# Kernel optimization log

Measured on AMD Instinct MI355X. Metric: run time of the kernel, lower is better.

## Reference

```python
import math
import jax, jax.numpy as jnp
import numpy as np

D = 4  # BWGNN d


def calculate_theta2(d):
    # Faithful numeric reimplementation of the sympy version.
    # f_i(x) = (x/2)^i (1-x/2)^(d-i) / (2*Beta(i+1, d+1-i)); the original code
    # keeps only the d lowest-order (ascending) coefficients, dropping x^d.
    thetas = []
    for i in range(d):
        c1 = np.zeros(i + 1); c1[i] = 0.5 ** i                      # (x/2)^i
        c2 = np.array([math.comb(d - i, j) * (-0.5) ** j
                       for j in range(d - i + 1)])                   # (1-x/2)^(d-i)
        c = np.convolve(c1, c2)                                      # ascending, len d+1
        B = math.factorial(i) * math.factorial(d - i) / math.factorial(d + 1)
        c = c / (2.0 * B)
        thetas.append([float(c[j]) for j in range(d)])               # coeff[d-i] slicing
    return thetas

THETAS = calculate_theta2(D)


def setup_inputs() -> dict:
    key = jax.random.key(0)
    k1, k2, k3, k4 = jax.random.split(key, 4)
    N, E, F_in, H = 100000, 1600000, 128, 64
    feature = jax.random.normal(k1, (N, F_in), dtype=jnp.float32)
    edge_index = jax.random.randint(k2, (2, E), 0, N, dtype=jnp.int32)
    W = jax.random.normal(k3, (F_in, H), dtype=jnp.float32) * 0.05
    b = jax.random.normal(k4, (H,), dtype=jnp.float32) * 0.05
    return {"feature": feature, "edge_index": edge_index, "W": W, "b": b}


def reference(feature, edge_index, W, b):
    N = feature.shape[0]
    src, dst = edge_index[0], edge_index[1]
    # out_degrees: number of out-edges per node (src side), clamped to >= 1
    deg = jax.ops.segment_sum(jnp.ones_like(src, dtype=jnp.float32), src,
                              num_segments=N)
    D_invsqrt = jnp.maximum(deg, 1.0) ** -0.5  # [N]
    D_invsqrt = D_invsqrt[:, None]             # [N,1]

    h = jax.nn.leaky_relu(feature @ W + b, negative_slope=0.01)  # [N,H]

    def unn_laplacian(feat):
        # feat - D^{-1/2} A^T D^{-1/2} feat  (copy_u + sum over dst)
        msg = (feat * D_invsqrt)[src]                          # [E,H]
        agg = jax.ops.segment_sum(msg, dst, num_segments=N)    # [N,H]
        return feat - agg * D_invsqrt

    outs = []
    for theta in THETAS:
        feat = h
        acc = theta[0] * feat
        for k in range(1, len(theta)):
            feat = unn_laplacian(feat)
            acc = acc + theta[k] * feat
        outs.append(acc)
    return jnp.concatenate(outs, axis=1)  # [N, len(THETAS)*H]
```

## Files before the change

kernel.cpp:

```cpp
#include <hip/hip_runtime.h>

#define THREADS 256
#define ELLW 64
#define T1 4096
#define BCAP 8192
#define NBMAX 512

__device__ __forceinline__ float bf2f(unsigned short u) {
    return __uint_as_float(((unsigned int)u) << 16);
}
__device__ __forceinline__ unsigned short f2bf(float x) {
    unsigned int u = __float_as_uint(x);
    u += 0x7fffu + ((u >> 16) & 1u);
    return (unsigned short)(u >> 16);
}

__global__ void bin_kernel(const int* __restrict__ key, const int* __restrict__ val,
                           int* __restrict__ gFill, unsigned int* __restrict__ gBuf, int E) {
    __shared__ int cnt[NBMAX], scanB[NBMAX], gbase[NBMAX], place[NBMAX];
    __shared__ unsigned int stage[T1];
    __shared__ unsigned int stageAddr[T1];
    const int tid = threadIdx.x;
    const int tileStart = blockIdx.x * T1;
    const int tileCnt = min(T1, E - tileStart);

    for (int i = tid; i < NBMAX; i += THREADS) { cnt[i] = 0; place[i] = 0; }
    __syncthreads();

    for (int i = tid; i < tileCnt; i += THREADS)
        atomicAdd(&cnt[key[tileStart + i] >> 8], 1);
    __syncthreads();

    if (tid < 64) {
        const int base = tid * 8;
        int loc[8]; int s = 0;
        #pragma unroll
        for (int k = 0; k < 8; ++k) { loc[k] = s; s += cnt[base + k]; }
        int run = s;
        #pragma unroll
        for (int off = 1; off < 64; off <<= 1) {
            int t = __shfl_up(run, off);
            if (tid >= off) run += t;
        }
        const int excl = run - s;
        #pragma unroll
        for (int k = 0; k < 8; ++k) scanB[base + k] = excl + loc[k];
    }
    __syncthreads();

    for (int i = tid; i < NBMAX; i += THREADS)
        gbase[i] = atomicAdd(&gFill[i], cnt[i]);
    __syncthreads();

    for (int i = tid; i < tileCnt; i += THREADS) {
        const int kk = key[tileStart + i];
        const int vv = val[tileStart + i];
        const int b = kk >> 8;
        const unsigned int rec = ((unsigned int)(kk & 255) << 17) | (unsigned int)vv;
        const int pos = atomicAdd(&place[b], 1);
        const int li = scanB[b] + pos;
        const int gi = gbase[b] + pos;
        stage[li] = rec;
        stageAddr[li] = (gi < BCAP) ? (unsigned int)(b * BCAP + gi) : 0xFFFFFFFFu;
    }
    __syncthreads();

    for (int i = tid; i < tileCnt; i += THREADS) {
        const unsigned int a = stageAddr[i];
        if (a != 0xFFFFFFFFu) gBuf[a] = stage[i];
    }
}

__global__ void ell_kernel(const int* __restrict__ gFill, const unsigned int* __restrict__ gBuf,
                           int* __restrict__ ell, int* __restrict__ fill, int N) {
    __shared__ int ellT[256 * ELLW];
    __shared__ int fillT[256];
    const int tid = threadIdx.x;
    const int b = blockIdx.x;
    const int nrec = min(gFill[b], BCAP);
    for (int i = tid; i < 256; i += THREADS) fillT[i] = 0;
    __syncthreads();
    for (int i = tid; i < nrec; i += THREADS) {
        const unsigned int rec = gBuf[(size_t)b * BCAP + i];
        const int dlow = rec >> 17;
        const int s = rec & 0x1FFFF;
        const int pos = atomicAdd(&fillT[dlow], 1);
        if (pos < ELLW) ellT[dlow * ELLW + pos] = s;
    }
    __syncthreads();
    const int node0 = b << 8;
    const int nvalid = min(256, N - node0);
    if (nvalid <= 0) return;
    for (int t = tid; t < nvalid; t += THREADS) fill[node0 + t] = min(fillT[t], ELLW);
    int4* dstp = (int4*)(ell + (size_t)node0 * ELLW);
    const int4* srcp = (const int4*)ellT;
    for (int i = tid; i < nvalid * 16; i += THREADS) dstp[i] = srcp[i];
}

__global__ void deg_kernel2(const int* __restrict__ gFill, const unsigned int* __restrict__ gBuf,
                            int* __restrict__ deg, int N) {
    __shared__ int cntT[256];
    const int tid = threadIdx.x;
    const int b = blockIdx.x;
    const int nrec = min(gFill[b], BCAP);
    for (int i = tid; i < 256; i += THREADS) cntT[i] = 0;
    __syncthreads();
    for (int i = tid; i < nrec; i += THREADS)
        atomicAdd(&cntT[gBuf[(size_t)b * BCAP + i] >> 17], 1);
    __syncthreads();
    const int node0 = b << 8;
    const int nvalid = min(256, N - node0);
    for (int t = tid; t < nvalid; t += THREADS) deg[node0 + t] = cntT[t];
}

__global__ void build_kernel(const int* __restrict__ src, const int* __restrict__ dst,
                             int* __restrict__ deg, int* __restrict__ fill,
                             int* __restrict__ ell, int E) {
    const int stride = gridDim.x * blockDim.x;
    for (int i = blockIdx.x * blockDim.x + threadIdx.x; i < E; i += stride) {
        const int s = src[i];
        const int d = dst[i];
        atomicAdd(&deg[s], 1);
        const int pos = atomicAdd(&fill[d], 1);
        if (pos < ELLW) ell[(size_t)d * ELLW + pos] = s;
    }
}

__global__ void gemm_leaky(const float* __restrict__ feat, const float* __restrict__ W,
                           const float* __restrict__ b, const int* __restrict__ deg,
                           float* __restrict__ out, int N) {
    __shared__ float Wl[128 * 64];
    __shared__ float fl[64][132];
    __shared__ float bl[64];

    {
        const float4* W4 = (const float4*)W;
        float4* Wl4 = (float4*)Wl;
        for (int i = threadIdx.x; i < 2048; i += THREADS) Wl4[i] = W4[i];
        if (threadIdx.x < 64) bl[threadIdx.x] = b[threadIdx.x];
    }

    const int cg = threadIdx.x & 15;
    const int rg = threadIdx.x >> 4;
    const int ntiles = (N + 63) >> 6;
    char* base = (char*)out;

    for (int tile = blockIdx.x; tile < ntiles; tile += gridDim.x) {
        const int n0 = tile << 6;
        __syncthreads();
        for (int i = threadIdx.x; i < 2048; i += THREADS) {
            int rr = i >> 5;
            int kk = i & 31;
            float4 v = make_float4(0.f, 0.f, 0.f, 0.f);
            if (n0 + rr < N) v = ((const float4*)(feat + (size_t)(n0 + rr) * 128))[kk];
            *((float4*)&fl[rr][kk * 4]) = v;
        }
        __syncthreads();

        float acc[4][4];
        #pragma unroll
        for (int j = 0; j < 4; ++j) {
            float bv = bl[cg * 4 + j];
            acc[0][j] = bv; acc[1][j] = bv; acc[2][j] = bv; acc[3][j] = bv;
        }

        #pragma unroll 4
        for (int k = 0; k < 128; ++k) {
            const float4 w = *((const float4*)&Wl[k * 64 + cg * 4]);
            const float f0 = fl[rg * 4 + 0][k];
            const float f1 = fl[rg * 4 + 1][k];
            const float f2 = fl[rg * 4 + 2][k];
            const float f3 = fl[rg * 4 + 3][k];
            acc[0][0] += f0 * w.x; acc[0][1] += f0 * w.y; acc[0][2] += f0 * w.z; acc[0][3] += f0 * w.w;
            acc[1][0] += f1 * w.x; acc[1][1] += f1 * w.y; acc[1][2] += f1 * w.z; acc[1][3] += f1 * w.w;
            acc[2][0] += f2 * w.x; acc[2][1] += f2 * w.y; acc[2][2] += f2 * w.z; acc[2][3] += f2 * w.w;
            acc[3][0] += f3 * w.x; acc[3][1] += f3 * w.y; acc[3][2] += f3 * w.z; acc[3][3] += f3 * w.w;
        }

        #pragma unroll
        for (int i = 0; i < 4; ++i) {
            const int n = n0 + rg * 4 + i;
            if (n < N) {
                const float dv = rsqrtf(fmaxf((float)deg[n], 1.0f));
                ushort4 o;
                float v0 = acc[i][0] > 0.f ? acc[i][0] : 0.01f * acc[i][0];
                float v1 = acc[i][1] > 0.f ? acc[i][1] : 0.01f * acc[i][1];
                float v2 = acc[i][2] > 0.f ? acc[i][2] : 0.01f * acc[i][2];
                float v3 = acc[i][3] > 0.f ? acc[i][3] : 0.01f * acc[i][3];
                o.x = f2bf(v0 * dv); o.y = f2bf(v1 * dv); o.z = f2bf(v2 * dv); o.w = f2bf(v3 * dv);
                *((ushort4*)(base + (size_t)n * 1024 + cg * 8)) = o;
            }
        }
    }
}

__global__ void hop_kernel(const int* __restrict__ ell, const int* __restrict__ fill,
                           const int* __restrict__ deg, float* __restrict__ out,
                           int N, int prevOff, int nextOff) {
    const int lane = threadIdx.x & 63;
    const int nwaves = (gridDim.x * blockDim.x) >> 6;
    char* base = (char*)out;
    for (int n = (blockIdx.x * blockDim.x + threadIdx.x) >> 6; n < N; n += nwaves) {
        const int cnt = min(fill[n], ELLW);
        const int c = ell[(size_t)n * ELLW + lane];
        float acc = 0.0f;
        int j = 0;
        for (; j + 4 <= cnt; j += 4) {
            const int s0 = __shfl(c, j);
            const int s1 = __shfl(c, j + 1);
            const int s2 = __shfl(c, j + 2);
            const int s3 = __shfl(c, j + 3);
            const float v0 = bf2f(*(const unsigned short*)(base + (size_t)s0 * 1024 + prevOff + lane * 2));
            const float v1 = bf2f(*(const unsigned short*)(base + (size_t)s1 * 1024 + prevOff + lane * 2));
            const float v2 = bf2f(*(const unsigned short*)(base + (size_t)s2 * 1024 + prevOff + lane * 2));
            const float v3 = bf2f(*(const unsigned short*)(base + (size_t)s3 * 1024 + prevOff + lane * 2));
            acc += (v0 + v1) + (v2 + v3);
        }
        for (; j < cnt; ++j) {
            const int s = __shfl(c, j);
            acc += bf2f(*(const unsigned short*)(base + (size_t)s * 1024 + prevOff + lane * 2));
        }
        const float own = bf2f(*(const unsigned short*)(base + (size_t)n * 1024 + prevOff + lane * 2));
        const float d = fmaxf((float)deg[n], 1.0f);
        const float sn = own - acc / d;
        *(unsigned short*)(base + (size_t)n * 1024 + nextOff + lane * 2) = f2bf(sn);
    }
}

__global__ void combine_kernel(float* __restrict__ out, const int* __restrict__ deg, int N) {
    const int lane = threadIdx.x & 63;
    const int nwaves = (gridDim.x * blockDim.x) >> 6;
    char* base = (char*)out;
    for (int n = (blockIdx.x * blockDim.x + threadIdx.x) >> 6; n < N; n += nwaves) {
        char* row = base + (size_t)n * 1024;
        const float s0 = bf2f(*(const unsigned short*)(row + 0   + lane * 2));
        const float s1 = bf2f(*(const unsigned short*)(row + 128 + lane * 2));
        const float s2 = bf2f(*(const unsigned short*)(row + 256 + lane * 2));
        const float s3 = bf2f(*(const unsigned short*)(row + 384 + lane * 2));
        const float sc = sqrtf(fmaxf((float)deg[n], 1.0f));
        const float h  = s0 * sc;
        const float p1 = s1 * sc;
        const float p2 = s2 * sc;
        const float p3 = s3 * sc;
        const float o0 = 2.5f * h - 5.0f * p1 + 3.75f * p2 - 1.25f * p3;
        const float o1 = 5.0f * p1 - 7.5f * p2 + 3.75f * p3;
        const float o2 = 3.75f * (p2 - p3);
        const float o3 = 1.25f * p3;
        float* frow = (float*)row;
        frow[lane]       = o0;
        frow[64 + lane]  = o1;
        frow[128 + lane] = o2;
        frow[192 + lane] = o3;
    }
}

extern "C" void kernel_launch(void* const* d_in, const int* in_sizes, int n_in,
                              void* d_out, int out_size, void* d_ws, size_t ws_size,
                              hipStream_t stream) {
    const float* feature = (const float*)d_in[0];
    const int*   eidx    = (const int*)d_in[1];
    const float* W       = (const float*)d_in[2];
    const float* b       = (const float*)d_in[3];
    float* out = (float*)d_out;

    const int N = in_sizes[0] / 128;
    const int E = in_sizes[1] / 2;
    const int* src = eidx;
    const int* dst = eidx + E;

    const int nb = (N + 255) >> 8;

    int* deg    = (int*)d_ws;
    int* fill   = deg + N;
    int* ell    = fill + N;
    int* gFillD = ell + (size_t)N * ELLW;
    int* gFillS = gFillD + NBMAX;
    unsigned int* gBufD = (unsigned int*)(gFillS + NBMAX);
    unsigned int* gBufS = gBufD + (size_t)nb * BCAP;

    if (N <= 131072) {
        hipMemsetAsync(gFillD, 0, 2 * NBMAX * sizeof(int), stream);
        const int tiles = (E + T1 - 1) / T1;
        bin_kernel<<<tiles, THREADS, 0, stream>>>(dst, src, gFillD, gBufD, E);
        bin_kernel<<<tiles, THREADS, 0, stream>>>(src, src, gFillS, gBufS, E);
        ell_kernel<<<nb, THREADS, 0, stream>>>(gFillD, gBufD, ell, fill, N);
        deg_kernel2<<<nb, THREADS, 0, stream>>>(gFillS, gBufS, deg, N);
    } else {
        hipMemsetAsync(deg, 0, (size_t)2 * N * sizeof(int), stream);
        build_kernel<<<2048, THREADS, 0, stream>>>(src, dst, deg, fill, ell, E);
    }

    const int gemm_blocks = (N + 63) / 64;
    gemm_leaky<<<gemm_blocks, THREADS, 0, stream>>>(feature, W, b, deg, out, N);

    const int gblocks = (N + 3) / 4;
    hop_kernel<<<gblocks, THREADS, 0, stream>>>(ell, fill, deg, out, N, 0, 128);
    hop_kernel<<<gblocks, THREADS, 0, stream>>>(ell, fill, deg, out, N, 128, 256);
    hop_kernel<<<gblocks, THREADS, 0, stream>>>(ell, fill, deg, out, N, 256, 384);

    combine_kernel<<<gblocks, THREADS, 0, stream>>>(out, deg, N);
}
```

Before: 269.4 us.

## Replace fixed-width ELL adjacency with compact CSR built via block scans

New measurement: 288.4 us. 1.07x slower.

```diff
diff --git a/kernel.cpp b/kernel.cpp
--- a/kernel.cpp
+++ b/kernel.cpp
@@ -1,7 +1,6 @@
 #include <hip/hip_runtime.h>
 
 #define THREADS 256
-#define ELLW 64
 #define T1 4096
 #define BCAP 8192
 #define NBMAX 512
@@ -13,6 +12,11 @@
     unsigned int u = __float_as_uint(x);
     u += 0x7fffu + ((u >> 16) & 1u);
     return (unsigned short)(u >> 16);
+}
+
+__global__ void zero_kernel(int* __restrict__ p, int n) {
+    const int i = blockIdx.x * blockDim.x + threadIdx.x;
+    if (i < n) p[i] = 0;
 }
 
 __global__ void bin_kernel(const int* __restrict__ key, const int* __restrict__ val,
@@ -71,30 +75,68 @@
     }
 }
 
-__global__ void ell_kernel(const int* __restrict__ gFill, const unsigned int* __restrict__ gBuf,
-                           int* __restrict__ ell, int* __restrict__ fill, int N) {
-    __shared__ int ellT[256 * ELLW];
-    __shared__ int fillT[256];
+__global__ void scanb_kernel(const int* __restrict__ gFill, int* __restrict__ gBase,
+                             int* __restrict__ rowptr, int nb, int N) {
+    __shared__ int s[NBMAX];
+    const int tid = threadIdx.x;
+    const int v = (tid < nb) ? min(gFill[tid], BCAP) : 0;
+    s[tid] = v;
+    __syncthreads();
+    for (int off = 1; off < NBMAX; off <<= 1) {
+        int t = (tid >= off) ? s[tid - off] : 0;
+        __syncthreads();
+        s[tid] += t;
+        __syncthreads();
+    }
+    if (tid < nb) gBase[tid] = s[tid] - v;
+    if (tid == NBMAX - 1) rowptr[N] = s[NBMAX - 1];
+}
+
+__global__ void csr_kernel(const int* __restrict__ gFill, const int* __restrict__ gBase,
+                           const unsigned int* __restrict__ gBuf,
+                           int* __restrict__ rowptr, int* __restrict__ col, int N) {
+    __shared__ int fillT[256], offT[256], place[256], sc[256];
+    __shared__ int colT[BCAP];
+    __shared__ int nwrite;
     const int tid = threadIdx.x;
     const int b = blockIdx.x;
     const int nrec = min(gFill[b], BCAP);
-    for (int i = tid; i < 256; i += THREADS) fillT[i] = 0;
-    __syncthreads();
+    const int base = gBase[b];
+
+    fillT[tid] = 0; place[tid] = 0;
+    __syncthreads();
+    for (int i = tid; i < nrec; i += THREADS)
+        atomicAdd(&fillT[gBuf[(size_t)b * BCAP + i] >> 17], 1);
+    __syncthreads();
+
+    int v = fillT[tid];
+    sc[tid] = v;
+    __syncthreads();
+    for (int off = 1; off < 256; off <<= 1) {
+        int t = (tid >= off) ? sc[tid - off] : 0;
+        __syncthreads();
+        sc[tid] += t;
+        __syncthreads();
+    }
+    offT[tid] = sc[tid] - v;
+    if (tid == 255) nwrite = sc[255];
+    __syncthreads();
+
+    const int node0 = b << 8;
+    const int nvalid = min(256, N - node0);
+    if (tid < nvalid) rowptr[node0 + tid] = base + offT[tid];
+
     for (int i = tid; i < nrec; i += THREADS) {
         const unsigned int rec = gBuf[(size_t)b * BCAP + i];
         const int dlow = rec >> 17;
         const int s = rec & 0x1FFFF;
-        const int pos = atomicAdd(&fillT[dlow], 1);
-        if (pos < ELLW) ellT[dlow * ELLW + pos] = s;
-    }
-    __syncthreads();
-    const int node0 = b << 8;
-    const int nvalid = min(256, N - node0);
-    if (nvalid <= 0) return;
-    for (int t = tid; t < nvalid; t += THREADS) fill[node0 + t] = min(fillT[t], ELLW);
-    int4* dstp = (int4*)(ell + (size_t)node0 * ELLW);
-    const int4* srcp = (const int4*)ellT;
-    for (int i = tid; i < nvalid * 16; i += THREADS) dstp[i] = srcp[i];
+        const int pos = atomicAdd(&place[dlow], 1);
+        colT[offT[dlow] + pos] = s;
+    }
+    __syncthreads();
+
+    const int nw = nwrite;
+    for (int i = tid; i < nw; i += THREADS) col[base + i] = colT[i];
 }
 
 __global__ void deg_kernel2(const int* __restrict__ gFill, const unsigned int* __restrict__ gBuf,
@@ -113,16 +155,45 @@
     for (int t = tid; t < nvalid; t += THREADS) deg[node0 + t] = cntT[t];
 }
 
-__global__ void build_kernel(const int* __restrict__ src, const int* __restrict__ dst,
-                             int* __restrict__ deg, int* __restrict__ fill,
-                             int* __restrict__ ell, int E) {
+__global__ void count_fb(const int* __restrict__ src, const int* __restrict__ dst,
+                         int* __restrict__ deg, int* __restrict__ cntd, int E) {
     const int stride = gridDim.x * blockDim.x;
     for (int i = blockIdx.x * blockDim.x + threadIdx.x; i < E; i += stride) {
-        const int s = src[i];
+        atomicAdd(&deg[src[i]], 1);
+        atomicAdd(&cntd[dst[i]], 1);
+    }
+}
+__global__ void scan_fb(const int* __restrict__ cnt, int* __restrict__ rowptr, int N) {
+    __shared__ int s[256];
+    __shared__ int carry;
+    const int tid = threadIdx.x;
+    if (tid == 0) carry = 0;
+    __syncthreads();
+    for (int basei = 0; basei < N; basei += 256) {
+        const int i = basei + tid;
+        const int v = (i < N) ? cnt[i] : 0;
+        s[tid] = v;
+        __syncthreads();
+        for (int off = 1; off < 256; off <<= 1) {
+            int t = (tid >= off) ? s[tid - off] : 0;
+            __syncthreads();
+            s[tid] += t;
+            __syncthreads();
+        }
+        if (i < N) rowptr[i] = carry + s[tid] - v;
+        __syncthreads();
+        if (tid == 0) carry += s[255];
+        __syncthreads();
+    }
+    if (tid == 0) rowptr[N] = carry;
+}
+__global__ void fill_fb(const int* __restrict__ src, const int* __restrict__ dst,
+                        const int* __restrict__ rowptr, int* __restrict__ place,
+                        int* __restrict__ col, int E) {
+    const int stride = gridDim.x * blockDim.x;
+    for (int i = blockIdx.x * blockDim.x + threadIdx.x; i < E; i += stride) {
         const int d = dst[i];
-        atomicAdd(&deg[s], 1);
-        const int pos = atomicAdd(&fill[d], 1);
-        if (pos < ELLW) ell[(size_t)d * ELLW + pos] = s;
+        col[rowptr[d] + atomicAdd(&place[d], 1)] = src[i];
     }
 }
 
@@ -194,31 +265,36 @@
     }
 }
 
-__global__ void hop_kernel(const int* __restrict__ ell, const int* __restrict__ fill,
+__global__ void hop_kernel(const int* __restrict__ rowptr, const int* __restrict__ col,
                            const int* __restrict__ deg, float* __restrict__ out,
                            int N, int prevOff, int nextOff) {
     const int lane = threadIdx.x & 63;
     const int nwaves = (gridDim.x * blockDim.x) >> 6;
     char* base = (char*)out;
     for (int n = (blockIdx.x * blockDim.x + threadIdx.x) >> 6; n < N; n += nwaves) {
-        const int cnt = min(fill[n], ELLW);
-        const int c = ell[(size_t)n * ELLW + lane];
+        const int beg = rowptr[n];
+        const int end = rowptr[n + 1];
         float acc = 0.0f;
-        int j = 0;
-        for (; j + 4 <= cnt; j += 4) {
-            const int s0 = __shfl(c, j);
-            const int s1 = __shfl(c, j + 1);
-            const int s2 = __shfl(c, j + 2);
-            const int s3 = __shfl(c, j + 3);
-            const float v0 = bf2f(*(const unsigned short*)(base + (size_t)s0 * 1024 + prevOff + lane * 2));
-            const float v1 = bf2f(*(const unsigned short*)(base + (size_t)s1 * 1024 + prevOff + lane * 2));
-            const float v2 = bf2f(*(const unsigned short*)(base + (size_t)s2 * 1024 + prevOff + lane * 2));
-            const float v3 = bf2f(*(const unsigned short*)(base + (size_t)s3 * 1024 + prevOff + lane * 2));
-            acc += (v0 + v1) + (v2 + v3);
-        }
-        for (; j < cnt; ++j) {
-            const int s = __shfl(c, j);
-            acc += bf2f(*(const unsigned short*)(base + (size_t)s * 1024 + prevOff + lane * 2));
+        for (int e0 = beg; e0 < end; e0 += 64) {
+            const int idx = e0 + lane;
+            const int c = (idx < end) ? col[idx] : 0;
+            const int m = min(64, end - e0);
+            int j = 0;
+            for (; j + 4 <= m; j += 4) {
+                const int s0 = __shfl(c, j);
+                const int s1 = __shfl(c, j + 1);
+                const int s2 = __shfl(c, j + 2);
+                const int s3 = __shfl(c, j + 3);
+                const float v0 = bf2f(*(const unsigned short*)(base + (size_t)s0 * 1024 + prevOff + lane * 2));
+                const float v1 = bf2f(*(const unsigned short*)(base + (size_t)s1 * 1024 + prevOff + lane * 2));
+                const float v2 = bf2f(*(const unsigned short*)(base + (size_t)s2 * 1024 + prevOff + lane * 2));
+                const float v3 = bf2f(*(const unsigned short*)(base + (size_t)s3 * 1024 + prevOff + lane * 2));
+                acc += (v0 + v1) + (v2 + v3);
+            }
+            for (; j < m; ++j) {
+                const int s = __shfl(c, j);
+                acc += bf2f(*(const unsigned short*)(base + (size_t)s * 1024 + prevOff + lane * 2));
+            }
         }
         const float own = bf2f(*(const unsigned short*)(base + (size_t)n * 1024 + prevOff + lane * 2));
         const float d = fmaxf((float)deg[n], 1.0f);
@@ -272,31 +348,37 @@
 
     int* deg    = (int*)d_ws;
     int* fill   = deg + N;
-    int* ell    = fill + N;
-    int* gFillD = ell + (size_t)N * ELLW;
+    int* rowptr = fill + N;
+    int* col    = rowptr + (N + 1);
+    int* gFillD = col + E;
     int* gFillS = gFillD + NBMAX;
-    unsigned int* gBufD = (unsigned int*)(gFillS + NBMAX);
+    int* gBase  = gFillS + NBMAX;
+    unsigned int* gBufD = (unsigned int*)(gBase + NBMAX);
     unsigned int* gBufS = gBufD + (size_t)nb * BCAP;
 
     if (N <= 131072) {
-        hipMemsetAsync(gFillD, 0, 2 * NBMAX * sizeof(int), stream);
+        zero_kernel<<<(2 * NBMAX + THREADS - 1) / THREADS, THREADS, 0, stream>>>(gFillD, 2 * NBMAX);
         const int tiles = (E + T1 - 1) / T1;
         bin_kernel<<<tiles, THREADS, 0, stream>>>(dst, src, gFillD, gBufD, E);
         bin_kernel<<<tiles, THREADS, 0, stream>>>(src, src, gFillS, gBufS, E);
-        ell_kernel<<<nb, THREADS, 0, stream>>>(gFillD, gBufD, ell, fill, N);
+        scanb_kernel<<<1, NBMAX, 0, stream>>>(gFillD, gBase, rowptr, nb, N);
+        csr_kernel<<<nb, THREADS, 0, stream>>>(gFillD, gBase, gBufD, rowptr, col, N);
         deg_kernel2<<<nb, THREADS, 0, stream>>>(gFillS, gBufS, deg, N);
     } else {
-        hipMemsetAsync(deg, 0, (size_t)2 * N * sizeof(int), stream);
-        build_kernel<<<2048, THREADS, 0, stream>>>(src, dst, deg, fill, ell, E);
+        zero_kernel<<<(2 * N + THREADS - 1) / THREADS, THREADS, 0, stream>>>(deg, 2 * N);
+        count_fb<<<2048, THREADS, 0, stream>>>(src, dst, deg, fill, E);
+        scan_fb<<<1, 256, 0, stream>>>(fill, rowptr, N);
+        zero_kernel<<<(N + THREADS - 1) / THREADS, THREADS, 0, stream>>>(fill, N);
+        fill_fb<<<2048, THREADS, 0, stream>>>(src, dst, rowptr, fill, col, E);
     }
 
     const int gemm_blocks = (N + 63) / 64;
     gemm_leaky<<<gemm_blocks, THREADS, 0, stream>>>(feature, W, b, deg, out, N);
 
     const int gblocks = (N + 3) / 4;
-    hop_kernel<<<gblocks, THREADS, 0, stream>>>(ell, fill, deg, out, N, 0, 128);
-    hop_kernel<<<gblocks, THREADS, 0, stream>>>(ell, fill, deg, out, N, 128, 256);
-    hop_kernel<<<gblocks, THREADS, 0, stream>>>(ell, fill, deg, out, N, 256, 384);
+    hop_kernel<<<gblocks, THREADS, 0, stream>>>(rowptr, col, deg, out, N, 0, 128);
+    hop_kernel<<<gblocks, THREADS, 0, stream>>>(rowptr, col, deg, out, N, 128, 256);
+    hop_kernel<<<gblocks, THREADS, 0, stream>>>(rowptr, col, deg, out, N, 256, 384);
 
     combine_kernel<<<gblocks, THREADS, 0, stream>>>(out, deg, N);
 }
```
